# Optimization experiments

Hardware: AMD Instinct MI355X
Metric: run time of the kernel (lower is better)

Reference implementation:

```python
import jax, jax.numpy as jnp
import numpy as np

DIM = 1024
EPS_LN = 1e-5
EPS_MEM = 1e-6

def _layernorm(x, g, b):
    mu = jnp.mean(x, axis=-1, keepdims=True)
    var = jnp.mean((x - mu) ** 2, axis=-1, keepdims=True)
    return (x - mu) * jax.lax.rsqrt(var + EPS_LN) * g + b

def setup_inputs() -> dict:
    key = jax.random.key(0)
    ks = jax.random.split(key, 8)
    B, S, D = 4, 4096, DIM
    s1 = 1.0 / np.sqrt(D)
    s2 = 1.0 / np.sqrt(4 * D)
    return {
        "x": jax.random.normal(ks[0], (B, S, D), dtype=jnp.float32),
        "ln1_g": jnp.ones((D,), jnp.float32),
        "ln1_b": jnp.zeros((D,), jnp.float32),
        "ln2_g": jnp.ones((D,), jnp.float32),
        "ln2_b": jnp.zeros((D,), jnp.float32),
        "gate_w": jax.random.uniform(ks[1], (D, D), jnp.float32, -s1, s1),
        "gate_b": jax.random.uniform(ks[2], (D,), jnp.float32, -s1, s1),
        "value_w": jax.random.uniform(ks[3], (D, D), jnp.float32, -s1, s1),
        "value_b": jax.random.uniform(ks[4], (D,), jnp.float32, -s1, s1),
        "ffn_w1": jax.random.uniform(ks[5], (D, 4 * D), jnp.float32, -s1, s1),
        "ffn_b1": jnp.zeros((4 * D,), jnp.float32),
        "ffn_w2": jax.random.uniform(ks[6], (4 * D, D), jnp.float32, -s2, s2),
        "ffn_b2": jnp.zeros((D,), jnp.float32),
    }

def reference(x, ln1_g, ln1_b, ln2_g, ln2_b, gate_w, gate_b, value_w, value_b, ffn_w1, ffn_b1, ffn_w2, ffn_b2):
    h = _layernorm(x, ln1_g, ln1_b)
    g = jax.nn.sigmoid(h @ gate_w + gate_b)
    v = h @ value_w + value_b
    cumsum_v = jnp.cumsum(g * v, axis=1)
    cumsum_g = jnp.cumsum(g, axis=1) + EPS_MEM
    x = x + cumsum_v / cumsum_g
    h2 = _layernorm(x, ln2_g, ln2_b)
    ffn = jax.nn.gelu(h2 @ ffn_w1 + ffn_b1, approximate=False) @ ffn_w2 + ffn_b2
    return x + ffn
```

## Files before the change

### kernel.cpp

```cpp
#include <hip/hip_runtime.h>
#include <cstdint>
#include <cstddef>

#define D_MODEL 1024
#define SEQ     4096
#define BATCH   4
#define M_ROWS  (BATCH*SEQ)
#define NCHUNK  64
#define LCHUNK  (SEQ/NCHUNK)

typedef __bf16 bf16_t;
typedef __bf16 bf16x8 __attribute__((ext_vector_type(8)));
typedef __bf16 bf16x4 __attribute__((ext_vector_type(4)));
typedef float  f32x4  __attribute__((ext_vector_type(4)));

__device__ __forceinline__ void load_lds_128(const bf16_t* g, bf16_t* l) {
    __builtin_amdgcn_global_load_lds(
        (const __attribute__((address_space(1))) unsigned int*)g,
        (__attribute__((address_space(3))) unsigned int*)l,
        16, 0, 0);
}

__device__ __forceinline__ float2 bf16pair_to_f2(unsigned int u) {
    union { unsigned int i; float f; } a, b;
    a.i = u << 16;
    b.i = u & 0xffff0000u;
    float2 r; r.x = a.f; r.y = b.f; return r;
}

__device__ __forceinline__ float gelu_f(float x) {
    float t = x * x;
    float u = x * (1.5957691216f + 0.07135481627f * t);
    return x / (1.0f + __expf(-u));
}

__global__ __launch_bounds__(256)
void transpose_all(const float* __restrict__ gate_w, const float* __restrict__ value_w,
                   const float* __restrict__ ffn_w1, const float* __restrict__ ffn_w2,
                   bf16_t* __restrict__ wgv_t, bf16_t* __restrict__ w1_t,
                   bf16_t* __restrict__ w2_t) {
    int id = blockIdx.x;
    const float* in; bf16_t* outp; int R, C, bx, by;
    if (id < 1024)      { in = gate_w;  outp = wgv_t;               R = 1024; C = 1024; bx = id & 31;  by = id >> 5; }
    else if (id < 2048) { id -= 1024; in = value_w; outp = wgv_t + 1024*1024; R = 1024; C = 1024; bx = id & 31;  by = id >> 5; }
    else if (id < 6144) { id -= 2048; in = ffn_w1;  outp = w1_t;    R = 1024; C = 4096; bx = id & 127; by = id >> 7; }
    else                { id -= 6144; in = ffn_w2;  outp = w2_t;    R = 4096; C = 1024; bx = id & 31;  by = id >> 5; }
    __shared__ float t[32][33];
    int tx = threadIdx.x & 31, ty = threadIdx.x >> 5;
    int c0 = bx * 32, r0 = by * 32;
    #pragma unroll
    for (int j = 0; j < 32; j += 8)
        t[ty + j][tx] = in[(size_t)(r0 + ty + j) * C + c0 + tx];
    __syncthreads();
    #pragma unroll
    for (int j = 0; j < 32; j += 8)
        outp[(size_t)(c0 + ty + j) * R + r0 + tx] = (bf16_t)t[tx][ty + j];
}

__global__ __launch_bounds__(256)
void ln_kernel(const float* __restrict__ x, const float* __restrict__ gamma,
               const float* __restrict__ beta, bf16_t* __restrict__ h) {
    int row = blockIdx.x;
    int tid = threadIdx.x;
    const float4* xr = (const float4*)(x + (size_t)row * D_MODEL);
    float4 v = xr[tid];
    float s  = v.x + v.y + v.z + v.w;
    float ss = v.x*v.x + v.y*v.y + v.z*v.z + v.w*v.w;
    #pragma unroll
    for (int off = 32; off; off >>= 1) {
        s  += __shfl_down(s, off);
        ss += __shfl_down(ss, off);
    }
    __shared__ float red[8];
    int wave = tid >> 6, lane = tid & 63;
    if (lane == 0) { red[wave] = s; red[4 + wave] = ss; }
    __syncthreads();
    if (tid == 0) {
        float S  = red[0] + red[1] + red[2] + red[3];
        float SS = red[4] + red[5] + red[6] + red[7];
        float mean = S * (1.0f / D_MODEL);
        float var  = SS * (1.0f / D_MODEL) - mean * mean;
        red[0] = mean;
        red[1] = rsqrtf(var + 1e-5f);
    }
    __syncthreads();
    float mean = red[0], rstd = red[1];
    float4 gv = ((const float4*)gamma)[tid];
    float4 bv = ((const float4*)beta)[tid];
    bf16x4 o;
    o[0] = (bf16_t)((v.x - mean) * rstd * gv.x + bv.x);
    o[1] = (bf16_t)((v.y - mean) * rstd * gv.y + bv.y);
    o[2] = (bf16_t)((v.z - mean) * rstd * gv.z + bv.z);
    o[3] = (bf16_t)((v.w - mean) * rstd * gv.w + bv.w);
    ((bf16x4*)h)[(size_t)row * (D_MODEL / 4) + tid] = o;
}

#define PHASE_MID() do { __builtin_amdgcn_s_barrier(); \
    asm volatile("s_waitcnt lgkmcnt(0)" ::: "memory"); \
    __builtin_amdgcn_s_setprio(1); } while (0)
#define PHASE_END() do { __builtin_amdgcn_s_setprio(0); \
    __builtin_amdgcn_s_barrier(); } while (0)
#define PHASE_END_VM() do { __builtin_amdgcn_s_setprio(0); \
    asm volatile("s_waitcnt vmcnt(4)" ::: "memory"); \
    __builtin_amdgcn_s_barrier(); } while (0)

#define LDA4(BUF, MB) do { _Pragma("unroll") for (int m_ = 0; m_ < 4; ++m_) { \
    af[m_][0] = *(const bf16x8*)((BUF) + aoff0 + ((MB)*4 + m_) * 1024); \
    af[m_][1] = *(const bf16x8*)((BUF) + aoff1 + ((MB)*4 + m_) * 1024); } } while (0)
#define LDB2(BUF, NLO) do { _Pragma("unroll") for (int n_ = 0; n_ < 2; ++n_) { \
    bfr[(NLO)+n_][0] = *(const bf16x8*)((BUF) + boff0 + ((NLO)+n_) * 1024); \
    bfr[(NLO)+n_][1] = *(const bf16x8*)((BUF) + boff1 + ((NLO)+n_) * 1024); } } while (0)
#define MFMA_HALF(MB, NLO) do { _Pragma("unroll") for (int m_ = 0; m_ < 4; ++m_) { \
    _Pragma("unroll") for (int n_ = 0; n_ < 2; ++n_) { \
        acc[(MB)*4 + m_][(NLO) + n_] = __builtin_amdgcn_mfma_f32_16x16x32_bf16( \
            bfr[(NLO)+n_][0], af[m_][0], acc[(MB)*4 + m_][(NLO) + n_], 0, 0, 0); \
        acc[(MB)*4 + m_][(NLO) + n_] = __builtin_amdgcn_mfma_f32_16x16x32_bf16( \
            bfr[(NLO)+n_][1], af[m_][1], acc[(MB)*4 + m_][(NLO) + n_], 0, 0, 0); } } } while (0)

template <int MODE, int TN, int TPB, int LKT>
__global__ __launch_bounds__(512, 2)
void gemm256(const bf16_t* __restrict__ A, const bf16_t* __restrict__ Bt,
             const float* __restrict__ bias, const float* __restrict__ bias2,
             const float* __restrict__ xres,
             void* __restrict__ out, void* __restrict__ out2,
             int M, int N, int K) {
    __shared__ __align__(16) bf16_t lds[2][2][256 * 64];

    const int KT = 1 << LKT;
    const int S  = TPB * KT;
    const int NI = S >> 1;

    const int tid  = threadIdx.x;
    const int lane = tid & 63;
    const int wave = tid >> 6;
    const int wm   = wave >> 2;
    const int wn   = wave & 3;

    const int L    = blockIdx.x;
    const int i    = L >> 3;
    const int ngrp = i & 3;
    const int mb   = (L & 7) + 8 * (i >> 2);
    const int m0   = mb * 256;
    const int n00  = ngrp * TPB * 256;

    f32x4 acc[8][4];
    #pragma unroll
    for (int ii = 0; ii < 8; ii++)
        #pragma unroll
        for (int j = 0; j < 4; j++) acc[ii][j] = (f32x4){0.f, 0.f, 0.f, 0.f};

    const int rr = tid >> 3;
    const int sc = ((tid & 7) ^ (rr & 7)) * 8;
    const bf16_t* pa0 = A  + ((size_t)(m0  + rr)) * K + sc;
    const bf16_t* pb0 = Bt + ((size_t)(n00 + rr)) * K + sc;
    const size_t rstep   = (size_t)64 * K;
    const size_t hstep   = rstep * 2;
    const size_t nstride = (size_t)256 * K;

    #define PA(s) (pa0 + (((s) & (KT - 1)) << 6))
    #define PB(s) (pb0 + (size_t)((s) >> LKT) * nstride + (((s) & (KT - 1)) << 6))

    const int l16 = lane & 15, quad = lane >> 4, swz = l16 & 7;
    const int aoff0 = (wm*128 + l16)*64 + ((quad    ) ^ swz)*8;
    const int aoff1 = (wm*128 + l16)*64 + ((quad + 4) ^ swz)*8;
    const int boff0 = (wn*64  + l16)*64 + ((quad    ) ^ swz)*8;
    const int boff1 = (wn*64  + l16)*64 + ((quad + 4) ^ swz)*8;

    bf16_t* LA0 = &lds[0][0][0]; bf16_t* LB0 = &lds[0][1][0];
    bf16_t* LA1 = &lds[1][0][0]; bf16_t* LB1 = &lds[1][1][0];

    auto STAGE = [&](const bf16_t* gsrc, bf16_t* dst) {
        load_lds_128(gsrc,         dst + tid * 8);
        load_lds_128(gsrc + rstep, dst + 4096 + tid * 8);
    };

    STAGE(PB(0),         LB0);
    STAGE(PB(0) + hstep, LB0 + 8192);
    STAGE(PA(0),         LA0);
    STAGE(PA(0) + hstep, LA0 + 8192);
    STAGE(PB(1),         LB1);
    STAGE(PB(1) + hstep, LB1 + 8192);
    asm volatile("s_waitcnt vmcnt(4)" ::: "memory");
    __builtin_amdgcn_s_barrier();

    #pragma unroll 1
    for (int it = 0; it < NI; ++it) {
        const int s1 = 2*it + 1;
        const int s2 = (2*it + 2 < S) ? 2*it + 2 : S - 1;
        const int s3 = (2*it + 3 < S) ? 2*it + 3 : S - 1;
        const bf16_t* a1 = PA(s1);
        const bf16_t* a2 = PA(s2);
        const bf16_t* b2 = PB(s2);
        const bf16_t* b3 = PB(s3);

        bf16x8 af[4][2], bfr[4][2];

        LDA4(LA0, 0); LDB2(LB0, 0);
        STAGE(a1, LA1);
        PHASE_MID(); MFMA_HALF(0, 0); PHASE_END();
        LDB2(LB0, 2);
        STAGE(a1 + hstep, LA1 + 8192);
        PHASE_MID(); MFMA_HALF(0, 2); PHASE_END();
        LDA4(LA0, 1);
        STAGE(b2, LB0);
        PHASE_MID(); MFMA_HALF(1, 0); PHASE_END();
        STAGE(b2 + hstep, LB0 + 8192);
        PHASE_MID(); MFMA_HALF(1, 2); PHASE_END_VM();
        LDA4(LA1, 0); LDB2(LB1, 0);
        STAGE(a2, LA0);
        PHASE_MID(); MFMA_HALF(0, 0); PHASE_END();
        LDB2(LB1, 2);
        STAGE(a2 + hstep, LA0 + 8192);
        PHASE_MID(); MFMA_HALF(0, 2); PHASE_END();
        LDA4(LA1, 1);
        STAGE(b3, LB1);
        PHASE_MID(); MFMA_HALF(1, 0); PHASE_END();
        STAGE(b3 + hstep, LB1 + 8192);
        PHASE_MID(); MFMA_HALF(1, 2); PHASE_END_VM();

        if (((it + 1) & ((KT >> 1) - 1)) == 0) {
            const int tdone = (2*it + 1) >> LKT;
            const int nn0 = n00 + tdone * 256;
            #pragma unroll
            for (int mt = 0; mt < 8; ++mt) {
                int row = m0 + wm * 128 + mt * 16 + l16;
                #pragma unroll
                for (int nt = 0; nt < 4; ++nt) {
                    int col = nn0 + wn * 64 + nt * 16 + quad * 4;
                    f32x4 a = acc[mt][nt];
                    if (MODE == 4) {
                        bool isV = (nn0 >= 1024);
                        int c1 = col & 1023;
                        float4 bv = *(const float4*)((isV ? bias2 : bias) + c1);
                        float4 val;
                        val.x = a[0] + bv.x; val.y = a[1] + bv.y;
                        val.z = a[2] + bv.z; val.w = a[3] + bv.w;
                        if (!isV) {
                            val.x = 1.0f / (1.0f + __expf(-val.x));
                            val.y = 1.0f / (1.0f + __expf(-val.y));
                            val.z = 1.0f / (1.0f + __expf(-val.z));
                            val.w = 1.0f / (1.0f + __expf(-val.w));
                        }
                        bf16x4 p;
                        p[0] = (bf16_t)val.x; p[1] = (bf16_t)val.y;
                        p[2] = (bf16_t)val.z; p[3] = (bf16_t)val.w;
                        bf16_t* o = (bf16_t*)(isV ? out2 : out);
                        *(bf16x4*)(o + (size_t)row * 1024 + c1) = p;
                    } else if (MODE == 2) {
                        float4 bv = *(const float4*)(bias + col);
                        bf16x4 p;
                        p[0] = (bf16_t)gelu_f(a[0] + bv.x);
                        p[1] = (bf16_t)gelu_f(a[1] + bv.y);
                        p[2] = (bf16_t)gelu_f(a[2] + bv.z);
                        p[3] = (bf16_t)gelu_f(a[3] + bv.w);
                        *(bf16x4*)((bf16_t*)out + (size_t)row * N + col) = p;
                    } else {
                        float4 bv = *(const float4*)(bias + col);
                        float4 xr = *(const float4*)(xres + (size_t)row * N + col);
                        float4 val;
                        val.x = xr.x + a[0] + bv.x; val.y = xr.y + a[1] + bv.y;
                        val.z = xr.z + a[2] + bv.z; val.w = xr.w + a[3] + bv.w;
                        *(float4*)((float*)out + (size_t)row * N + col) = val;
                    }
                    acc[mt][nt] = (f32x4){0.f, 0.f, 0.f, 0.f};
                }
            }
        }
    }

    asm volatile("s_waitcnt vmcnt(0)" ::: "memory");
    #undef PA
    #undef PB
}

__global__ __launch_bounds__(128)
void scan_partial(const bf16_t* __restrict__ g, const bf16_t* __restrict__ v,
                  float* __restrict__ sg, float* __restrict__ sgv) {
    int dt = blockIdx.x & 1;
    int c  = (blockIdx.x >> 1) & (NCHUNK - 1);
    int b  = blockIdx.x >> 7;
    int d  = dt * 512 + threadIdx.x * 4;
    float s0 = 0.f, s1 = 0.f, s2 = 0.f, s3 = 0.f;
    float t0 = 0.f, t1 = 0.f, t2 = 0.f, t3 = 0.f;
    #pragma unroll 4
    for (int i = 0; i < LCHUNK; i++) {
        size_t idx = ((size_t)(b * SEQ + c * LCHUNK + i)) * D_MODEL + d;
        uint2 gu = *(const uint2*)(g + idx);
        uint2 vu = *(const uint2*)(v + idx);
        float2 ga = bf16pair_to_f2(gu.x), gb = bf16pair_to_f2(gu.y);
        float2 va = bf16pair_to_f2(vu.x), vb = bf16pair_to_f2(vu.y);
        s0 += ga.x; s1 += ga.y; s2 += gb.x; s3 += gb.y;
        t0 += ga.x * va.x; t1 += ga.y * va.y;
        t2 += gb.x * vb.x; t3 += gb.y * vb.y;
    }
    size_t o = ((size_t)(b * NCHUNK + c)) * D_MODEL + d;
    *(float4*)(sg + o)  = make_float4(s0, s1, s2, s3);
    *(float4*)(sgv + o) = make_float4(t0, t1, t2, t3);
}

__global__ __launch_bounds__(128)
void scan_apply(const bf16_t* __restrict__ g, const bf16_t* __restrict__ v,
                const float* __restrict__ x, const float* __restrict__ sg,
                const float* __restrict__ sgv, float* __restrict__ out) {
    int dt = blockIdx.x & 1;
    int c  = (blockIdx.x >> 1) & (NCHUNK - 1);
    int b  = blockIdx.x >> 7;
    int d  = dt * 512 + threadIdx.x * 4;
    float rg0 = 0.f, rg1 = 0.f, rg2 = 0.f, rg3 = 0.f;
    float rv0 = 0.f, rv1 = 0.f, rv2 = 0.f, rv3 = 0.f;
    for (int p = 0; p < c; p++) {
        size_t o = ((size_t)(b * NCHUNK + p)) * D_MODEL + d;
        float4 a  = *(const float4*)(sg + o);
        float4 bb = *(const float4*)(sgv + o);
        rg0 += a.x;  rg1 += a.y;  rg2 += a.z;  rg3 += a.w;
        rv0 += bb.x; rv1 += bb.y; rv2 += bb.z; rv3 += bb.w;
    }
    #pragma unroll 2
    for (int i = 0; i < LCHUNK; i++) {
        size_t idx = ((size_t)(b * SEQ + c * LCHUNK + i)) * D_MODEL + d;
        uint2 gu = *(const uint2*)(g + idx);
        uint2 vu = *(const uint2*)(v + idx);
        float2 ga = bf16pair_to_f2(gu.x), gb = bf16pair_to_f2(gu.y);
        float2 va = bf16pair_to_f2(vu.x), vb = bf16pair_to_f2(vu.y);
        rg0 += ga.x; rv0 += ga.x * va.x;
        rg1 += ga.y; rv1 += ga.y * va.y;
        rg2 += gb.x; rv2 += gb.x * vb.x;
        rg3 += gb.y; rv3 += gb.y * vb.y;
        float4 xv = *(const float4*)(x + idx);
        float4 ov;
        ov.x = xv.x + rv0 / (rg0 + 1e-6f);
        ov.y = xv.y + rv1 / (rg1 + 1e-6f);
        ov.z = xv.z + rv2 / (rg2 + 1e-6f);
        ov.w = xv.w + rv3 / (rg3 + 1e-6f);
        *(float4*)(out + idx) = ov;
    }
}

extern "C" void kernel_launch(void* const* d_in, const int* in_sizes, int n_in,
                              void* d_out, int out_size, void* d_ws, size_t ws_size,
                              hipStream_t stream) {
    (void)in_sizes; (void)n_in; (void)out_size; (void)ws_size;
    const float* x       = (const float*)d_in[0];
    const float* ln1_g   = (const float*)d_in[1];
    const float* ln1_b   = (const float*)d_in[2];
    const float* ln2_g   = (const float*)d_in[3];
    const float* ln2_b   = (const float*)d_in[4];
    const float* gate_w  = (const float*)d_in[5];
    const float* gate_b  = (const float*)d_in[6];
    const float* value_w = (const float*)d_in[7];
    const float* value_b = (const float*)d_in[8];
    const float* ffn_w1  = (const float*)d_in[9];
    const float* ffn_b1  = (const float*)d_in[10];
    const float* ffn_w2  = (const float*)d_in[11];
    const float* ffn_b2  = (const float*)d_in[12];
    float* out = (float*)d_out;

    char* ws = (char*)d_ws;
    const size_t MB = 1024 * 1024;
    bf16_t* wgv_t = (bf16_t*)(ws + 0 * MB);
    bf16_t* w1_t  = (bf16_t*)(ws + 4 * MB);
    bf16_t* w2_t  = (bf16_t*)(ws + 12 * MB);
    bf16_t* h     = (bf16_t*)(ws + 20 * MB);
    bf16_t* g     = (bf16_t*)(ws + 52 * MB);
    bf16_t* v     = (bf16_t*)(ws + 84 * MB);
    float*  sg    = (float*)(ws + 116 * MB);
    float*  sgv   = (float*)(ws + 117 * MB);
    bf16_t* act   = (bf16_t*)(ws + 118 * MB);

    transpose_all<<<10240, 256, 0, stream>>>(gate_w, value_w, ffn_w1, ffn_w2,
                                             wgv_t, w1_t, w2_t);

    ln_kernel<<<M_ROWS, 256, 0, stream>>>(x, ln1_g, ln1_b, h);

    gemm256<4, 8, 2, 4><<<256, 512, 0, stream>>>(
        h, wgv_t, gate_b, value_b, nullptr, g, v, M_ROWS, 2048, 1024);

    scan_partial<<<BATCH * NCHUNK * 2, 128, 0, stream>>>(g, v, sg, sgv);
    scan_apply<<<BATCH * NCHUNK * 2, 128, 0, stream>>>(g, v, x, sg, sgv, out);

    ln_kernel<<<M_ROWS, 256, 0, stream>>>(out, ln2_g, ln2_b, h);

    gemm256<2, 16, 4, 4><<<256, 512, 0, stream>>>(
        h, w1_t, ffn_b1, nullptr, nullptr, act, nullptr, M_ROWS, 4096, 1024);

    gemm256<3, 4, 1, 6><<<256, 512, 0, stream>>>(
        act, w2_t, ffn_b2, nullptr, out, out, nullptr, M_ROWS, 1024, 4096);
}
```

Before: 596.3 us.

## Restructure GEMM main loop barrier schedule and load all B fragments at once

Rewrites the inner K-loop schedule of the 256x256 bf16 GEMM: barriers drop from two per MFMA half-phase to one, all four B fragments are loaded from LDS together, and the lgkmcnt waits are placed after MFMA batches instead of before them. The aim is less barrier stall and better overlap of LDS reads and global-to-LDS staging with MFMA work. In exchange, more fragments stay live in registers, and the reordered waits and barriers risk LDS read/write hazards on the double buffers if the ordering is subtly wrong.

Result: faster. 570.2 us (-4.4%).

```diff
diff --git a/kernel.cpp b/kernel.cpp
--- a/kernel.cpp
+++ b/kernel.cpp
@@ -95,21 +95,19 @@
     ((bf16x4*)h)[(size_t)row * (D_MODEL / 4) + tid] = o;
 }
 
-#define PHASE_MID() do { __builtin_amdgcn_s_barrier(); \
-    asm volatile("s_waitcnt lgkmcnt(0)" ::: "memory"); \
-    __builtin_amdgcn_s_setprio(1); } while (0)
-#define PHASE_END() do { __builtin_amdgcn_s_setprio(0); \
-    __builtin_amdgcn_s_barrier(); } while (0)
-#define PHASE_END_VM() do { __builtin_amdgcn_s_setprio(0); \
-    asm volatile("s_waitcnt vmcnt(4)" ::: "memory"); \
-    __builtin_amdgcn_s_barrier(); } while (0)
+#define FENCE() asm volatile("" ::: "memory")
+#define BAR() do { FENCE(); __builtin_amdgcn_s_barrier(); FENCE(); } while (0)
+#define LGKM0() asm volatile("s_waitcnt lgkmcnt(0)" ::: "memory")
+#define VMW4() asm volatile("s_waitcnt vmcnt(4)" ::: "memory")
+#define PRIO1() __builtin_amdgcn_s_setprio(1)
+#define PRIO0() __builtin_amdgcn_s_setprio(0)
 
 #define LDA4(BUF, MB) do { _Pragma("unroll") for (int m_ = 0; m_ < 4; ++m_) { \
     af[m_][0] = *(const bf16x8*)((BUF) + aoff0 + ((MB)*4 + m_) * 1024); \
     af[m_][1] = *(const bf16x8*)((BUF) + aoff1 + ((MB)*4 + m_) * 1024); } } while (0)
-#define LDB2(BUF, NLO) do { _Pragma("unroll") for (int n_ = 0; n_ < 2; ++n_) { \
-    bfr[(NLO)+n_][0] = *(const bf16x8*)((BUF) + boff0 + ((NLO)+n_) * 1024); \
-    bfr[(NLO)+n_][1] = *(const bf16x8*)((BUF) + boff1 + ((NLO)+n_) * 1024); } } while (0)
+#define LDB4(BUF) do { _Pragma("unroll") for (int n_ = 0; n_ < 4; ++n_) { \
+    bfr[n_][0] = *(const bf16x8*)((BUF) + boff0 + n_ * 1024); \
+    bfr[n_][1] = *(const bf16x8*)((BUF) + boff1 + n_ * 1024); } } while (0)
 #define MFMA_HALF(MB, NLO) do { _Pragma("unroll") for (int m_ = 0; m_ < 4; ++m_) { \
     _Pragma("unroll") for (int n_ = 0; n_ < 2; ++n_) { \
         acc[(MB)*4 + m_][(NLO) + n_] = __builtin_amdgcn_mfma_f32_16x16x32_bf16( \
@@ -180,8 +178,8 @@
     STAGE(PA(0) + hstep, LA0 + 8192);
     STAGE(PB(1),         LB1);
     STAGE(PB(1) + hstep, LB1 + 8192);
-    asm volatile("s_waitcnt vmcnt(4)" ::: "memory");
-    __builtin_amdgcn_s_barrier();
+    VMW4();
+    BAR();
 
     #pragma unroll 1
     for (int it = 0; it < NI; ++it) {
@@ -195,28 +193,36 @@
 
         bf16x8 af[4][2], bfr[4][2];
 
-        LDA4(LA0, 0); LDB2(LB0, 0);
         STAGE(a1, LA1);
-        PHASE_MID(); MFMA_HALF(0, 0); PHASE_END();
-        LDB2(LB0, 2);
+        VMW4();
+        BAR();
+        LDA4(LA0, 0); LDB4(LB0);
+        PRIO1(); MFMA_HALF(0, 0); PRIO0(); LGKM0();
         STAGE(a1 + hstep, LA1 + 8192);
-        PHASE_MID(); MFMA_HALF(0, 2); PHASE_END();
+        BAR();
+        PRIO1(); MFMA_HALF(0, 2); PRIO0();
+        STAGE(b2, LB0);
+        BAR();
         LDA4(LA0, 1);
-        STAGE(b2, LB0);
-        PHASE_MID(); MFMA_HALF(1, 0); PHASE_END();
+        PRIO1(); MFMA_HALF(1, 0); PRIO0(); LGKM0();
         STAGE(b2 + hstep, LB0 + 8192);
-        PHASE_MID(); MFMA_HALF(1, 2); PHASE_END_VM();
-        LDA4(LA1, 0); LDB2(LB1, 0);
+        BAR();
+        PRIO1(); MFMA_HALF(1, 2); PRIO0();
         STAGE(a2, LA0);
-        PHASE_MID(); MFMA_HALF(0, 0); PHASE_END();
-        LDB2(LB1, 2);
+        VMW4();
+        BAR();
+        LDA4(LA1, 0); LDB4(LB1);
+        PRIO1(); MFMA_HALF(0, 0); PRIO0(); LGKM0();
         STAGE(a2 + hstep, LA0 + 8192);
-        PHASE_MID(); MFMA_HALF(0, 2); PHASE_END();
+        BAR();
+        PRIO1(); MFMA_HALF(0, 2); PRIO0();
+        STAGE(b3, LB1);
+        BAR();
         LDA4(LA1, 1);
-        STAGE(b3, LB1);
-        PHASE_MID(); MFMA_HALF(1, 0); PHASE_END();
+        PRIO1(); MFMA_HALF(1, 0); PRIO0(); LGKM0();
         STAGE(b3 + hstep, LB1 + 8192);
-        PHASE_MID(); MFMA_HALF(1, 2); PHASE_END_VM();
+        BAR();
+        PRIO1(); MFMA_HALF(1, 2); PRIO0();
 
         if (((it + 1) & ((KT >> 1) - 1)) == 0) {
             const int tdone = (2*it + 1) >> LKT;
```
